# Performance work log

Hardware: AMD Instinct MI355X
Metric: run time of the kernel (lower is better)

Reference implementation:

```python
import jax, jax.numpy as jnp
import numpy as np

N = 8192          # nodes in batch
D_IN = 512        # in_channels
G = 512           # global_dim
D_OUT = 512       # out_channels
H = 8             # heads
C = 2048          # num_centroids
NUM_NODES = 100000


def setup_inputs() -> dict:
    key = jax.random.key(0)
    ks = jax.random.split(key, 10)
    s = lambda fan_in: 1.0 / np.sqrt(fan_in)
    return {
        "x": jax.random.normal(ks[0], (N, D_IN), jnp.float32),
        "W_proj": jax.random.normal(ks[1], (D_IN, G), jnp.float32) * s(D_IN),
        "b_proj": jnp.zeros((G,), jnp.float32),
        "W_q": jax.random.normal(ks[2], (G, D_OUT), jnp.float32) * s(G),
        "b_q": jnp.zeros((D_OUT,), jnp.float32),
        "W_k": jax.random.normal(ks[3], (G, D_OUT), jnp.float32) * s(G),
        "b_k": jnp.zeros((D_OUT,), jnp.float32),
        "W_v": jax.random.normal(ks[4], (G, D_OUT), jnp.float32) * s(G),
        "b_v": jnp.zeros((D_OUT,), jnp.float32),
        "k_buf": jax.random.normal(ks[5], (C, G), jnp.float32),
        "v_buf": jax.random.normal(ks[6], (C, G), jnp.float32),
        "ln_gamma": jnp.ones((D_OUT,), jnp.float32),
        "ln_beta": jnp.zeros((D_OUT,), jnp.float32),
        "c_idx": jax.random.randint(ks[7], (NUM_NODES,), 0, C, jnp.int64 if jax.config.jax_enable_x64 else jnp.int32),
        "node_indices": jax.random.randint(ks[8], (N,), 0, NUM_NODES, jnp.int64 if jax.config.jax_enable_x64 else jnp.int32),
    }


def _layer_norm(y, gamma, beta, eps=1e-5):
    mu = jnp.mean(y, axis=-1, keepdims=True)
    var = jnp.var(y, axis=-1, keepdims=True)
    return (y - mu) * jax.lax.rsqrt(var + eps) * gamma + beta


def reference(x, W_proj, b_proj, W_q, b_q, W_k, b_k, W_v, b_v,
              k_buf, v_buf, ln_gamma, ln_beta, c_idx, node_indices):
    h, d = H, D_OUT
    dh = d // h
    scale = 1.0 / np.sqrt(d)  # source scales by 1/sqrt(out_channels)

    q_x = x @ W_proj + b_proj                      # [N, G]
    k_x = jax.lax.stop_gradient(k_buf)             # detach().clone()
    v_x = jax.lax.stop_gradient(v_buf)

    # n (h d) -> h n d
    q = (q_x @ W_q + b_q).reshape(-1, h, dh).transpose(1, 0, 2)   # [h, N, dh]
    k = (k_x @ W_k + b_k).reshape(-1, h, dh).transpose(1, 0, 2)   # [h, C, dh]
    v = (v_x @ W_v + b_v).reshape(-1, h, dh).transpose(1, 0, 2)   # [h, C, dh]

    dots = jnp.einsum('hnd,hcd->hnc', q, k) * scale               # [h, N, C]

    # log-count centroid bias (unique/bincount over the full c_idx buffer)
    counts = jnp.bincount(c_idx, length=C)                        # [C] int
    dots = dots + jnp.log(counts.astype(dots.dtype))              # log(0)=-inf masks empty centroids

    attn = jax.nn.softmax(dots, axis=-1)                          # [h, N, C]
    out = jnp.einsum('hnc,hcd->hnd', attn, v)                     # [h, N, dh]
    out = out.transpose(1, 0, 2).reshape(-1, d)                   # [N, d]

    return _layer_norm(out, ln_gamma, ln_beta)
```

## Files before the change

kernel.cpp:

```cpp
#include <hip/hip_runtime.h>
#include <math.h>

typedef __bf16 bf16x8 __attribute__((ext_vector_type(8)));
typedef __bf16 bf16x2 __attribute__((ext_vector_type(2)));
typedef float f32x4 __attribute__((ext_vector_type(4)));
typedef float f32x16 __attribute__((ext_vector_type(16)));
typedef unsigned u32x2v __attribute__((ext_vector_type(2)));
typedef unsigned short u16;

#define NQ 8192
#define DMODEL 512
#define NHEAD 8
#define DH 64
#define NC 2048
#define NIDX 100000

__device__ __forceinline__ u16 f2bf(float f) {
    unsigned u = __float_as_uint(f);
    u += 0x7fffu + ((u >> 16) & 1u);
    return (u16)(u >> 16);
}
__device__ __forceinline__ float bf2f(u16 h) {
    return __uint_as_float(((unsigned)h) << 16);
}
__device__ __forceinline__ unsigned pk2(float a, float b) {
    bf16x2 t; t[0] = (__bf16)a; t[1] = (__bf16)b;
    return __builtin_bit_cast(unsigned, t);
}
__device__ __forceinline__ void plswap(unsigned& a, unsigned& b) {
    u32x2v r = __builtin_amdgcn_permlane32_swap(a, b, false, false);
    a = r[0]; b = r[1];
}
__device__ __forceinline__ int soff(int q, int col) {
    return q * 256 + ((((col >> 2) ^ (q & 7)) << 2) | (col & 3));
}

__global__ __launch_bounds__(256) void k_prep(
    const float* __restrict__ x, const float* __restrict__ kb, const float* __restrict__ vb,
    const float* __restrict__ Wp, const float* __restrict__ Wq, const float* __restrict__ Wk,
    const float* __restrict__ Wv, const float* __restrict__ bp, const float* __restrict__ bq_,
    const int* __restrict__ cidx,
    u16* __restrict__ x_bf, u16* __restrict__ kb_bf, u16* __restrict__ vb_bf,
    u16* __restrict__ Wp_bf, u16* __restrict__ Wq_t, u16* __restrict__ Wk_t,
    u16* __restrict__ Wv_t, int* __restrict__ counts, float* __restrict__ bcomb)
{
    __shared__ float tile[32][33];
    int bid = blockIdx.x, tid = threadIdx.x;
    if (bid < 6400) {
        const float* src; u16* dst; int i;
        if (bid < 4096)      { src = x;  dst = x_bf;  i = bid; }
        else if (bid < 5120) { src = kb; dst = kb_bf; i = bid - 4096; }
        else if (bid < 6144) { src = vb; dst = vb_bf; i = bid - 5120; }
        else                 { src = Wp; dst = Wp_bf; i = bid - 6144; }
        int e = (i * 256 + tid) * 4;
        float4 v = *(const float4*)(src + e);
        ushort4 o;
        o.x = f2bf(v.x); o.y = f2bf(v.y); o.z = f2bf(v.z); o.w = f2bf(v.w);
        *(ushort4*)(dst + e) = o;
    } else if (bid < 7168) {
        const float* W; u16* Wt; int tb;
        if (bid < 6656)      { W = Wq; Wt = Wq_t; tb = bid - 6400; }
        else if (bid < 6912) { W = Wk; Wt = Wk_t; tb = bid - 6656; }
        else                 { W = Wv; Wt = Wv_t; tb = bid - 6912; }
        int c0 = (tb & 15) * 32, r0 = (tb >> 4) * 32;
        int tx = tid & 31, ty = tid >> 5;
#pragma unroll
        for (int i = 0; i < 4; i++)
            tile[ty + i * 8][tx] = W[(size_t)(r0 + ty + i * 8) * DMODEL + c0 + tx];
        __syncthreads();
#pragma unroll
        for (int i = 0; i < 4; i++)
            Wt[(size_t)(c0 + ty + i * 8) * DMODEL + r0 + tx] = f2bf(tile[tx][ty + i * 8]);
    } else if (bid < 7296) {
        for (int i = (bid - 7168) * 256 + tid; i < NIDX; i += 128 * 256)
            atomicAdd(&counts[cidx[i]], 1);
    } else {
        int j = (bid - 7296) * 256 + tid;
        float s = bq_[j];
        for (int k = 0; k < DMODEL; k++) s += bp[k] * Wq[(size_t)k * DMODEL + j];
        bcomb[j] = s;
    }
}

template <int OUT_T>
__device__ __forceinline__ void gemm_bt_body(
    const u16* __restrict__ A, const u16* __restrict__ Bt,
    const float* __restrict__ bias, u16* __restrict__ Cmat,
    int M, int N, int K, int bx, int by)
{
    constexpr int LDP = 40;
    __shared__ __align__(16) u16 As[128 * LDP];
    __shared__ __align__(16) u16 Bs[128 * LDP];
    int tid = threadIdx.x;
    int lane = tid & 63, wid = tid >> 6;
    int wrow = (wid >> 1) * 64, wcol = (wid & 1) * 64;
    int m0 = by * 128, n0 = bx * 128;
    int lr = lane & 15, lg = lane >> 4;
    f32x4 acc[4][4] = {};

    for (int k0 = 0; k0 < K; k0 += 32) {
#pragma unroll
        for (int c = 0; c < 2; c++) {
            int ch = tid + c * 256;
            int row = ch >> 2, colc = (ch & 3) * 8;
            uint4 av = *(const uint4*)(A + (size_t)(m0 + row) * K + k0 + colc);
            *(uint4*)(&As[row * LDP + colc]) = av;
            uint4 bv = *(const uint4*)(Bt + (size_t)(n0 + row) * K + k0 + colc);
            *(uint4*)(&Bs[row * LDP + colc]) = bv;
        }
        __syncthreads();
        bf16x8 af[4], bfr[4];
#pragma unroll
        for (int m = 0; m < 4; m++)
            af[m] = *(const bf16x8*)(&As[(wrow + m * 16 + lr) * LDP + lg * 8]);
#pragma unroll
        for (int n = 0; n < 4; n++)
            bfr[n] = *(const bf16x8*)(&Bs[(wcol + n * 16 + lr) * LDP + lg * 8]);
#pragma unroll
        for (int m = 0; m < 4; m++)
#pragma unroll
            for (int n = 0; n < 4; n++)
                acc[m][n] = __builtin_amdgcn_mfma_f32_16x16x32_bf16(af[m], bfr[n], acc[m][n], 0, 0, 0);
        __syncthreads();
    }
#pragma unroll
    for (int n = 0; n < 4; n++) {
        int col = n0 + wcol + n * 16 + lr;
        float bv = bias ? bias[col] : 0.0f;
#pragma unroll
        for (int m = 0; m < 4; m++) {
            int rbase = m0 + wrow + m * 16 + lg * 4;
            if (OUT_T == 1) {
                int hh = col >> 6, T = (col >> 5) & 1, ql = col & 31;
                int t = rbase >> 5, cc = rbase & 31;
                int u = ((cc >> 4) * 2 + ((cc >> 3) & 1)) * 2 + T;
                size_t off = (size_t)hh * 131072 + (size_t)t * 2048 + u * 256 + ql * 8 + (cc & 7);
                ushort4 o4;
                o4.x = f2bf(acc[m][n][0] + bv);
                o4.y = f2bf(acc[m][n][1] + bv);
                o4.z = f2bf(acc[m][n][2] + bv);
                o4.w = f2bf(acc[m][n][3] + bv);
                *(ushort4*)(Cmat + off) = o4;
            } else if (OUT_T == 2) {
                int hh = col >> 6, m2 = (col >> 4) & 3, h2 = (col >> 3) & 1, jj = col & 7;
                size_t ub = (size_t)hh * 131072 + (size_t)(m2 * 2 + h2) * 256 + jj;
#pragma unroll
                for (int r = 0; r < 4; r++) {
                    int c = rbase + r;
                    Cmat[ub + (size_t)(c >> 5) * 2048 + (c & 31) * 8] = f2bf(acc[m][n][r] + bv);
                }
            } else {
#pragma unroll
                for (int r = 0; r < 4; r++)
                    Cmat[(size_t)(rbase + r) * N + col] = f2bf(acc[m][n][r] + bv);
            }
        }
    }
}

template <int OUT_T>
__global__ __launch_bounds__(256) void k_gemm_bt(
    const u16* __restrict__ A, const u16* __restrict__ Bt,
    const float* __restrict__ bias, u16* __restrict__ Cmat, int M, int N, int K)
{
    gemm_bt_body<OUT_T>(A, Bt, bias, Cmat, M, N, K, blockIdx.x, blockIdx.y);
}

__global__ __launch_bounds__(256) void k_gemm_kv(
    const u16* __restrict__ Ak, const u16* __restrict__ Wkt, const float* __restrict__ bk,
    u16* __restrict__ Kp,
    const u16* __restrict__ Av, const u16* __restrict__ Wvt, const float* __restrict__ bv,
    u16* __restrict__ Vp)
{
    if (blockIdx.z == 0)
        gemm_bt_body<2>(Ak, Wkt, bk, Kp, NC, DMODEL, DMODEL, blockIdx.x, blockIdx.y);
    else
        gemm_bt_body<1>(Av, Wvt, bv, Vp, NC, DMODEL, DMODEL, blockIdx.x, blockIdx.y);
}

__global__ __launch_bounds__(512, 2) void k_attn8(
    const u16* __restrict__ Q, const u16* __restrict__ Kp, const u16* __restrict__ Vp,
    const int* __restrict__ counts, const float* __restrict__ ln_g,
    const float* __restrict__ ln_b, float* __restrict__ Out, float scale2)
{
    __shared__ float sbias[NC];
    __shared__ unsigned sO[32 * 256];

    int tid = threadIdx.x;
    int lane = tid & 63, wid = tid >> 6;
    int h = wid;
    int ql = lane & 31, hi = lane >> 5;
    int q0 = blockIdx.x * 32;
    int hbase = h * DH;

#pragma unroll
    for (int i = 0; i < 4; i++)
        sbias[tid + i * 512] = log2f((float)counts[tid + i * 512]) - 16.0f;

    bf16x8 qf[4];
#pragma unroll
    for (int m = 0; m < 4; m++)
        qf[m] = *(const bf16x8*)(Q + (size_t)(q0 + ql) * DMODEL + hbase + m * 16 + hi * 8);

    const u16* klane = Kp + (size_t)h * 131072 + hi * 256 + ql * 8;
    const u16* vlane = Vp + (size_t)h * 131072 + hi * 512 + ql * 8;

    bf16x8 kf0[4], kf1[4], vf0[4], vf1[4];
#pragma unroll
    for (int m = 0; m < 4; m++)
        kf0[m] = *(const bf16x8*)(klane + m * 512);
#pragma unroll
    for (int T = 0; T < 2; T++)
#pragma unroll
        for (int ss = 0; ss < 2; ss++)
            vf0[T * 2 + ss] = *(const bf16x8*)(vlane + ss * 1024 + T * 256);

    f32x16 o0 = {}, o1 = {};
    float l_part = 0.f;

    __syncthreads();

    auto body = [&](int t, bf16x8 (&kfc)[4], bf16x8 (&vfc)[4],
                    bf16x8 (&kfn)[4], bf16x8 (&vfn)[4]) {
        const u16* kp = klane + (size_t)(t + 1) * 2048;
        const u16* vp = vlane + (size_t)(t + 1) * 2048;
#pragma unroll
        for (int m = 0; m < 4; m++)
            kfn[m] = *(const bf16x8*)(kp + m * 512);
#pragma unroll
        for (int T = 0; T < 2; T++)
#pragma unroll
            for (int ss = 0; ss < 2; ss++)
                vfn[T * 2 + ss] = *(const bf16x8*)(vp + ss * 1024 + T * 256);

        f32x4 bq[4];
#pragma unroll
        for (int j = 0; j < 4; j++)
            bq[j] = *(const f32x4*)(sbias + t * 32 + 8 * j + 4 * hi);

        f32x16 acc = {};
        __builtin_amdgcn_s_setprio(1);
#pragma unroll
        for (int m = 0; m < 4; m++)
            acc = __builtin_amdgcn_mfma_f32_32x32x16_bf16(kfc[m], qf[m], acc, 0, 0, 0);
        __builtin_amdgcn_s_setprio(0);

        unsigned u[8];
        float rs0 = 0.f, rs1 = 0.f;
#pragma unroll
        for (int j = 0; j < 8; j++) {
            float p0 = exp2f(acc[2 * j] * scale2 + bq[(2 * j) >> 2][(2 * j) & 3]);
            float p1 = exp2f(acc[2 * j + 1] * scale2 + bq[(2 * j + 1) >> 2][(2 * j + 1) & 3]);
            rs0 += p0; rs1 += p1;
            u[j] = pk2(p0, p1);
        }
        l_part += rs0 + rs1;

        plswap(u[0], u[2]); plswap(u[1], u[3]);
        plswap(u[4], u[6]); plswap(u[5], u[7]);
        bf16x8 pb0 = __builtin_bit_cast(bf16x8, *(uint4*)&u[0]);
        bf16x8 pb1 = __builtin_bit_cast(bf16x8, *(uint4*)&u[4]);

        __builtin_amdgcn_s_setprio(1);
        o0 = __builtin_amdgcn_mfma_f32_32x32x16_bf16(vfc[0], pb0, o0, 0, 0, 0);
        o0 = __builtin_amdgcn_mfma_f32_32x32x16_bf16(vfc[1], pb1, o0, 0, 0, 0);
        o1 = __builtin_amdgcn_mfma_f32_32x32x16_bf16(vfc[2], pb0, o1, 0, 0, 0);
        o1 = __builtin_amdgcn_mfma_f32_32x32x16_bf16(vfc[3], pb1, o1, 0, 0, 0);
        __builtin_amdgcn_s_setprio(0);
    };

    for (int t = 0; t < NC / 32; t += 2) {
        body(t,     kf0, vf0, kf1, vf1);
        body(t + 1, kf1, vf1, kf0, vf0);
    }

    float l_tot = l_part + __shfl_xor(l_part, 32);
    float inv = 1.0f / l_tot;

#pragma unroll
    for (int T = 0; T < 2; T++)
#pragma unroll
        for (int j = 0; j < 8; j++) {
            int dw = T * 16 + (j & 1) + 4 * (j >> 1) + 2 * hi;
            float a = (T == 0) ? o0[2 * j] : o1[2 * j];
            float b = (T == 0) ? o0[2 * j + 1] : o1[2 * j + 1];
            sO[soff(ql, h * 32 + dw)] = pk2(a * inv, b * inv);
        }
    __syncthreads();

    float4 g0 = *(const float4*)(ln_g + lane * 8);
    float4 g1 = *(const float4*)(ln_g + lane * 8 + 4);
    float4 b0 = *(const float4*)(ln_b + lane * 8);
    float4 b1 = *(const float4*)(ln_b + lane * 8 + 4);
#pragma unroll
    for (int rr = 0; rr < 4; rr++) {
        int r = wid * 4 + rr;
        uint4 pw = *(const uint4*)(&sO[r * 256 + ((lane ^ (r & 7)) << 2)]);
        float v[8];
        v[0] = bf2f((u16)(pw.x & 0xffff)); v[1] = bf2f((u16)(pw.x >> 16));
        v[2] = bf2f((u16)(pw.y & 0xffff)); v[3] = bf2f((u16)(pw.y >> 16));
        v[4] = bf2f((u16)(pw.z & 0xffff)); v[5] = bf2f((u16)(pw.z >> 16));
        v[6] = bf2f((u16)(pw.w & 0xffff)); v[7] = bf2f((u16)(pw.w >> 16));
        float sum = 0.f, sq = 0.f;
#pragma unroll
        for (int j = 0; j < 8; j++) { sum += v[j]; sq += v[j] * v[j]; }
#pragma unroll
        for (int msk = 1; msk <= 32; msk <<= 1) { sum += __shfl_xor(sum, msk); sq += __shfl_xor(sq, msk); }
        float mu = sum * (1.f / DMODEL);
        float var = sq * (1.f / DMODEL) - mu * mu;
        float rstd = rsqrtf(var + 1e-5f);
        float o[8];
        o[0] = (v[0] - mu) * rstd * g0.x + b0.x; o[1] = (v[1] - mu) * rstd * g0.y + b0.y;
        o[2] = (v[2] - mu) * rstd * g0.z + b0.z; o[3] = (v[3] - mu) * rstd * g0.w + b0.w;
        o[4] = (v[4] - mu) * rstd * g1.x + b1.x; o[5] = (v[5] - mu) * rstd * g1.y + b1.y;
        o[6] = (v[6] - mu) * rstd * g1.z + b1.z; o[7] = (v[7] - mu) * rstd * g1.w + b1.w;
        float* op = Out + (size_t)(q0 + r) * DMODEL + lane * 8;
        *(float4*)op = *(float4*)&o[0];
        *(float4*)(op + 4) = *(float4*)&o[4];
    }
}

extern "C" void kernel_launch(void* const* d_in, const int* in_sizes, int n_in,
                              void* d_out, int out_size, void* d_ws, size_t ws_size,
                              hipStream_t stream)
{
    const float* x      = (const float*)d_in[0];
    const float* W_proj = (const float*)d_in[1];
    const float* b_proj = (const float*)d_in[2];
    const float* W_q    = (const float*)d_in[3];
    const float* b_q    = (const float*)d_in[4];
    const float* W_k    = (const float*)d_in[5];
    const float* b_k    = (const float*)d_in[6];
    const float* W_v    = (const float*)d_in[7];
    const float* b_v    = (const float*)d_in[8];
    const float* k_buf  = (const float*)d_in[9];
    const float* v_buf  = (const float*)d_in[10];
    const float* ln_g   = (const float*)d_in[11];
    const float* ln_b   = (const float*)d_in[12];
    const int*   c_idx  = (const int*)d_in[13];
    float* out = (float*)d_out;

    char* ws = (char*)d_ws;
    size_t off = 0;
    auto alloc = [&](size_t bytes) -> void* {
        void* p = ws + off;
        off += (bytes + 255) & ~(size_t)255;
        return p;
    };
    u16* x_bf   = (u16*)alloc((size_t)NQ * DMODEL * 2);
    u16* kb_bf  = (u16*)alloc((size_t)NC * DMODEL * 2);
    u16* vb_bf  = (u16*)alloc((size_t)NC * DMODEL * 2);
    u16* Wp_bf  = (u16*)alloc((size_t)DMODEL * DMODEL * 2);
    u16* Wq_t   = (u16*)alloc((size_t)DMODEL * DMODEL * 2);
    u16* Wk_t   = (u16*)alloc((size_t)DMODEL * DMODEL * 2);
    u16* Wv_t   = (u16*)alloc((size_t)DMODEL * DMODEL * 2);
    u16* WcombT = (u16*)alloc((size_t)DMODEL * DMODEL * 2);
    u16* Qm     = (u16*)alloc((size_t)NQ * DMODEL * 2);
    u16* Kpm    = (u16*)alloc((size_t)NC * DMODEL * 2);
    u16* Vpm    = (u16*)alloc((size_t)DMODEL * NC * 2);
    int*   counts = (int*)alloc(NC * 4);
    float* bcomb  = (float*)alloc(DMODEL * 4);
    (void)alloc(262144);

    hipMemsetAsync(counts, 0, NC * 4, stream);

    k_prep<<<dim3(7298), dim3(256), 0, stream>>>(
        x, k_buf, v_buf, W_proj, W_q, W_k, W_v, b_proj, b_q, c_idx,
        x_bf, kb_bf, vb_bf, Wp_bf, Wq_t, Wk_t, Wv_t, counts, bcomb);

    k_gemm_bt<0><<<dim3(4, 4), dim3(256), 0, stream>>>(Wq_t, Wp_bf, nullptr, WcombT, DMODEL, DMODEL, DMODEL);
    k_gemm_kv<<<dim3(4, 16, 2), dim3(256), 0, stream>>>(kb_bf, Wk_t, b_k, Kpm,
                                                        vb_bf, Wv_t, b_v, Vpm);
    k_gemm_bt<0><<<dim3(4, 64), dim3(256), 0, stream>>>(x_bf, WcombT, bcomb, Qm, NQ, DMODEL, DMODEL);

    k_attn8<<<dim3(NQ / 32), dim3(512), 0, stream>>>(Qm, Kpm, Vpm, counts, ln_g, ln_b, out, 0.06375872f);
    (void)in_sizes; (void)n_in; (void)out_size; (void)ws_size;
}
```

Measured before the change: 143.4 us.

## Fuse fp32-to-bf16 conversion into GEMM loads and merge K/V/Q GEMMs

```diff
diff --git a/kernel.cpp b/kernel.cpp
--- a/kernel.cpp
+++ b/kernel.cpp
@@ -35,33 +35,26 @@
     return q * 256 + ((((col >> 2) ^ (q & 7)) << 2) | (col & 3));
 }
 
-__global__ __launch_bounds__(256) void k_prep(
-    const float* __restrict__ x, const float* __restrict__ kb, const float* __restrict__ vb,
+__global__ __launch_bounds__(256) void k_prep2(
     const float* __restrict__ Wp, const float* __restrict__ Wq, const float* __restrict__ Wk,
     const float* __restrict__ Wv, const float* __restrict__ bp, const float* __restrict__ bq_,
     const int* __restrict__ cidx,
-    u16* __restrict__ x_bf, u16* __restrict__ kb_bf, u16* __restrict__ vb_bf,
     u16* __restrict__ Wp_bf, u16* __restrict__ Wq_t, u16* __restrict__ Wk_t,
     u16* __restrict__ Wv_t, int* __restrict__ counts, float* __restrict__ bcomb)
 {
     __shared__ float tile[32][33];
     int bid = blockIdx.x, tid = threadIdx.x;
-    if (bid < 6400) {
-        const float* src; u16* dst; int i;
-        if (bid < 4096)      { src = x;  dst = x_bf;  i = bid; }
-        else if (bid < 5120) { src = kb; dst = kb_bf; i = bid - 4096; }
-        else if (bid < 6144) { src = vb; dst = vb_bf; i = bid - 5120; }
-        else                 { src = Wp; dst = Wp_bf; i = bid - 6144; }
-        int e = (i * 256 + tid) * 4;
-        float4 v = *(const float4*)(src + e);
+    if (bid < 256) {
+        int e = (bid * 256 + tid) * 4;
+        float4 v = *(const float4*)(Wp + e);
         ushort4 o;
         o.x = f2bf(v.x); o.y = f2bf(v.y); o.z = f2bf(v.z); o.w = f2bf(v.w);
-        *(ushort4*)(dst + e) = o;
-    } else if (bid < 7168) {
+        *(ushort4*)(Wp_bf + e) = o;
+    } else if (bid < 1024) {
         const float* W; u16* Wt; int tb;
-        if (bid < 6656)      { W = Wq; Wt = Wq_t; tb = bid - 6400; }
-        else if (bid < 6912) { W = Wk; Wt = Wk_t; tb = bid - 6656; }
-        else                 { W = Wv; Wt = Wv_t; tb = bid - 6912; }
+        if (bid < 512)       { W = Wq; Wt = Wq_t; tb = bid - 256; }
+        else if (bid < 768)  { W = Wk; Wt = Wk_t; tb = bid - 512; }
+        else                 { W = Wv; Wt = Wv_t; tb = bid - 768; }
         int c0 = (tb & 15) * 32, r0 = (tb >> 4) * 32;
         int tx = tid & 31, ty = tid >> 5;
 #pragma unroll
@@ -71,20 +64,20 @@
 #pragma unroll
         for (int i = 0; i < 4; i++)
             Wt[(size_t)(c0 + ty + i * 8) * DMODEL + r0 + tx] = f2bf(tile[tx][ty + i * 8]);
-    } else if (bid < 7296) {
-        for (int i = (bid - 7168) * 256 + tid; i < NIDX; i += 128 * 256)
+    } else if (bid < 1152) {
+        for (int i = (bid - 1024) * 256 + tid; i < NIDX; i += 128 * 256)
             atomicAdd(&counts[cidx[i]], 1);
     } else {
-        int j = (bid - 7296) * 256 + tid;
+        int j = (bid - 1152) * 256 + tid;
         float s = bq_[j];
         for (int k = 0; k < DMODEL; k++) s += bp[k] * Wq[(size_t)k * DMODEL + j];
         bcomb[j] = s;
     }
 }
 
-template <int OUT_T>
+template <int A_F32, int OUT_T>
 __device__ __forceinline__ void gemm_bt_body(
-    const u16* __restrict__ A, const u16* __restrict__ Bt,
+    const void* __restrict__ A_, const u16* __restrict__ Bt,
     const float* __restrict__ bias, u16* __restrict__ Cmat,
     int M, int N, int K, int bx, int by)
 {
@@ -103,7 +96,16 @@
         for (int c = 0; c < 2; c++) {
             int ch = tid + c * 256;
             int row = ch >> 2, colc = (ch & 3) * 8;
-            uint4 av = *(const uint4*)(A + (size_t)(m0 + row) * K + k0 + colc);
+            uint4 av;
+            if (A_F32) {
+                const float* Af = (const float*)A_;
+                float4 a0 = *(const float4*)(Af + (size_t)(m0 + row) * K + k0 + colc);
+                float4 a1 = *(const float4*)(Af + (size_t)(m0 + row) * K + k0 + colc + 4);
+                av.x = pk2(a0.x, a0.y); av.y = pk2(a0.z, a0.w);
+                av.z = pk2(a1.x, a1.y); av.w = pk2(a1.z, a1.w);
+            } else {
+                av = *(const uint4*)((const u16*)A_ + (size_t)(m0 + row) * K + k0 + colc);
+            }
             *(uint4*)(&As[row * LDP + colc]) = av;
             uint4 bv = *(const uint4*)(Bt + (size_t)(n0 + row) * K + k0 + colc);
             *(uint4*)(&Bs[row * LDP + colc]) = bv;
@@ -158,24 +160,27 @@
     }
 }
 
-template <int OUT_T>
-__global__ __launch_bounds__(256) void k_gemm_bt(
-    const u16* __restrict__ A, const u16* __restrict__ Bt,
-    const float* __restrict__ bias, u16* __restrict__ Cmat, int M, int N, int K)
-{
-    gemm_bt_body<OUT_T>(A, Bt, bias, Cmat, M, N, K, blockIdx.x, blockIdx.y);
-}
-
-__global__ __launch_bounds__(256) void k_gemm_kv(
-    const u16* __restrict__ Ak, const u16* __restrict__ Wkt, const float* __restrict__ bk,
+__global__ __launch_bounds__(256) void k_gemm_wc(
+    const u16* __restrict__ A, const u16* __restrict__ Bt, u16* __restrict__ Cmat)
+{
+    gemm_bt_body<0, 0>(A, Bt, nullptr, Cmat, DMODEL, DMODEL, DMODEL, blockIdx.x, blockIdx.y);
+}
+
+__global__ __launch_bounds__(256) void k_gemm_all(
+    const float* __restrict__ kb, const u16* __restrict__ Wkt, const float* __restrict__ bk,
     u16* __restrict__ Kp,
-    const u16* __restrict__ Av, const u16* __restrict__ Wvt, const float* __restrict__ bv,
-    u16* __restrict__ Vp)
-{
-    if (blockIdx.z == 0)
-        gemm_bt_body<2>(Ak, Wkt, bk, Kp, NC, DMODEL, DMODEL, blockIdx.x, blockIdx.y);
+    const float* __restrict__ vb, const u16* __restrict__ Wvt, const float* __restrict__ bv,
+    u16* __restrict__ Vp,
+    const float* __restrict__ x, const u16* __restrict__ WcombT,
+    const float* __restrict__ bcomb, u16* __restrict__ Qm)
+{
+    int b = blockIdx.x;
+    if (b < 64)
+        gemm_bt_body<1, 2>(kb, Wkt, bk, Kp, NC, DMODEL, DMODEL, b & 3, b >> 2);
+    else if (b < 128)
+        gemm_bt_body<1, 1>(vb, Wvt, bv, Vp, NC, DMODEL, DMODEL, (b - 64) & 3, (b - 64) >> 2);
     else
-        gemm_bt_body<1>(Av, Wvt, bv, Vp, NC, DMODEL, DMODEL, blockIdx.x, blockIdx.y);
+        gemm_bt_body<1, 0>(x, WcombT, bcomb, Qm, NQ, DMODEL, DMODEL, (b - 128) & 3, (b - 128) >> 2);
 }
 
 __global__ __launch_bounds__(512, 2) void k_attn8(
@@ -347,9 +352,6 @@
         off += (bytes + 255) & ~(size_t)255;
         return p;
     };
-    u16* x_bf   = (u16*)alloc((size_t)NQ * DMODEL * 2);
-    u16* kb_bf  = (u16*)alloc((size_t)NC * DMODEL * 2);
-    u16* vb_bf  = (u16*)alloc((size_t)NC * DMODEL * 2);
     u16* Wp_bf  = (u16*)alloc((size_t)DMODEL * DMODEL * 2);
     u16* Wq_t   = (u16*)alloc((size_t)DMODEL * DMODEL * 2);
     u16* Wk_t   = (u16*)alloc((size_t)DMODEL * DMODEL * 2);
@@ -364,14 +366,16 @@
 
     hipMemsetAsync(counts, 0, NC * 4, stream);
 
-    k_prep<<<dim3(7298), dim3(256), 0, stream>>>(
-        x, k_buf, v_buf, W_proj, W_q, W_k, W_v, b_proj, b_q, c_idx,
-        x_bf, kb_bf, vb_bf, Wp_bf, Wq_t, Wk_t, Wv_t, counts, bcomb);
-
-    k_gemm_bt<0><<<dim3(4, 4), dim3(256), 0, stream>>>(Wq_t, Wp_bf, nullptr, WcombT, DMODEL, DMODEL, DMODEL);
-    k_gemm_kv<<<dim3(4, 16, 2), dim3(256), 0, stream>>>(kb_bf, Wk_t, b_k, Kpm,
-                                                        vb_bf, Wv_t, b_v, Vpm);
-    k_gemm_bt<0><<<dim3(4, 64), dim3(256), 0, stream>>>(x_bf, WcombT, bcomb, Qm, NQ, DMODEL, DMODEL);
+    k_prep2<<<dim3(1154), dim3(256), 0, stream>>>(
+        W_proj, W_q, W_k, W_v, b_proj, b_q, c_idx,
+        Wp_bf, Wq_t, Wk_t, Wv_t, counts, bcomb);
+
+    k_gemm_wc<<<dim3(4, 4), dim3(256), 0, stream>>>(Wq_t, Wp_bf, WcombT);
+
+    k_gemm_all<<<dim3(384), dim3(256), 0, stream>>>(
+        k_buf, Wk_t, b_k, Kpm,
+        v_buf, Wv_t, b_v, Vpm,
+        x, WcombT, bcomb, Qm);
 
     k_attn8<<<dim3(NQ / 32), dim3(512), 0, stream>>>(Qm, Kpm, Vpm, counts, ln_g, ln_b, out, 0.06375872f);
     (void)in_sizes; (void)n_in; (void)out_size; (void)ws_size;
```

After: 136.8 us. 1.05x faster.
